# Optimization experiments

Hardware: AMD Instinct MI355X
Metric: run time of the kernel (lower is better)

The kernel has to match this reference:

```python
import jax, jax.numpy as jnp
import numpy as np


def _rope(x, token_positions, theta):
    # x: [B, H, S, D], token_positions: [S]
    d = x.shape[-1]
    freqs = 1.0 / theta ** (jnp.arange(0, d, 2, dtype=jnp.float32) / d)  # [D/2]
    angles = token_positions.astype(jnp.float32)[:, None] * freqs[None, :]  # [S, D/2]
    cos, sin = jnp.cos(angles), jnp.sin(angles)
    x_even = x[..., 0::2]
    x_odd = x[..., 1::2]
    new_even = x_even * cos - x_odd * sin
    new_odd = x_even * sin + x_odd * cos
    return jnp.stack([new_even, new_odd], axis=-1).reshape(x.shape)


def setup_inputs() -> dict:
    key = jax.random.key(0)
    ks = jax.random.split(key, 5)
    B, S, D = 2, 2048, 1024
    scale = 1.0 / np.sqrt(D)
    return {
        "x": jax.random.normal(ks[0], (B, S, D), dtype=jnp.float32),
        "Wq": jax.random.normal(ks[1], (D, D), dtype=jnp.float32) * scale,
        "Wk": jax.random.normal(ks[2], (D, D), dtype=jnp.float32) * scale,
        "Wv": jax.random.normal(ks[3], (D, D), dtype=jnp.float32) * scale,
        "Wo": jax.random.normal(ks[4], (D, D), dtype=jnp.float32) * scale,
        "token_positions": jnp.arange(S, dtype=jnp.int32),
        "rope_theta": 10000,
    }


def reference(x, Wq, Wk, Wv, Wo, token_positions, rope_theta):
    B, S, Dm = x.shape
    H = 16
    d_k = Dm // H
    # nn.Linear(bias=False): y = x @ W.T
    def proj(W):
        y = jnp.einsum('bsd,ed->bse', x, W)
        return y.reshape(B, S, H, d_k).transpose(0, 2, 1, 3)  # [B,H,S,Dk]
    q = _rope(proj(Wq), token_positions, float(rope_theta))
    k = _rope(proj(Wk), token_positions, float(rope_theta))
    v = proj(Wv)
    scores = jnp.einsum('bhqd,bhkd->bhqk', q, k) / jnp.sqrt(jnp.float32(d_k))
    causal = jnp.tril(jnp.ones((S, S), dtype=bool))
    scores = jnp.where(causal, scores, -jnp.inf)
    p = jax.nn.softmax(scores, axis=-1)
    vals = jnp.einsum('bhqk,bhkd->bhqd', p, v)
    out = vals.transpose(0, 2, 1, 3).reshape(B, S, Dm)
    return jnp.einsum('bsd,ed->bse', out, Wo)
```

## Files before the change

kernel.cpp:

```cpp
#include <hip/hip_runtime.h>
#include <hip/hip_bf16.h>
#include <stdint.h>

typedef __attribute__((ext_vector_type(8))) __bf16 bf16x8;
typedef __attribute__((ext_vector_type(4))) float f32x4;
typedef __hip_bfloat16 bf16;

#define GLDS(g, l) __builtin_amdgcn_global_load_lds( \
    (const __attribute__((address_space(1))) void*)(g), \
    (__attribute__((address_space(3))) void*)(l), 16, 0, 0)

#define SCALE_Q 0.18033688f

#define OFF_XB     ((size_t)0)
#define OFF_WQKVB  ((size_t)8388608)
#define OFF_WOB    ((size_t)14680064)
#define OFF_QB     ((size_t)16777216)
#define OFF_KB     ((size_t)25165824)
#define OFF_VTB    ((size_t)33554432)
#define OFF_CS     ((size_t)41943040)
#define OFF_SN     ((size_t)42205184)

__global__ void prep_kernel(const float* __restrict__ x, const float* __restrict__ wq,
                            const float* __restrict__ wk, const float* __restrict__ wv,
                            const float* __restrict__ wo,
                            bf16* __restrict__ xb, bf16* __restrict__ wqkvb,
                            bf16* __restrict__ wob)
{
    const int region = blockIdx.y;
    const float* src;
    bf16* dst;
    int count;
    switch (region) {
        case 0:  src = x;  dst = xb;              count = 4096 * 1024; break;
        case 1:  src = wq; dst = wqkvb;           count = 1024 * 1024; break;
        case 2:  src = wk; dst = wqkvb + 1048576; count = 1024 * 1024; break;
        case 3:  src = wv; dst = wqkvb + 2097152; count = 1024 * 1024; break;
        default: src = wo; dst = wob;             count = 1024 * 1024; break;
    }
    const int i = (blockIdx.x * 256 + threadIdx.x) * 4;
    if (i >= count) return;
    const float4 v = *(const float4*)(src + i);
    union { bf16 h[4]; short4 s4; } u;
    u.h[0] = __float2bfloat16(v.x);
    u.h[1] = __float2bfloat16(v.y);
    u.h[2] = __float2bfloat16(v.z);
    u.h[3] = __float2bfloat16(v.w);
    *(short4*)(dst + i) = u.s4;
}

__global__ void rope_table_kernel(const int* __restrict__ pos, const void* __restrict__ theta_p,
                                  float* __restrict__ cst, float* __restrict__ snt)
{
    const int t = blockIdx.x * 256 + threadIdx.x;
    const int s = t >> 5, i = t & 31;
    const int ti = ((const int*)theta_p)[0];
    const float theta = (ti > 0 && ti < 100000000) ? (float)ti : ((const float*)theta_p)[0];
    const float fr = expf(-(float)i * (1.0f / 32.0f) * logf(theta));
    const float ang = (float)pos[s] * fr;
    cst[t] = cosf(ang);
    snt[t] = sinf(ang);
}

template<int MODE, int BM>
__global__ __launch_bounds__(256) void gemm_bt(
    const bf16* __restrict__ A, const bf16* __restrict__ B,
    const int K, const int N,
    float* __restrict__ outf,
    bf16* __restrict__ qb, bf16* __restrict__ kb, bf16* __restrict__ vtb,
    const float* __restrict__ cst, const float* __restrict__ snt)
{
    constexpr int NF = BM / 32;
    __shared__ __align__(16) bf16 Asl[BM * 64];
    __shared__ __align__(16) bf16 Bsl[128 * 64];
    const int tid = threadIdx.x;
    const int wave = tid >> 6, lane = tid & 63;
    const int lr = lane & 15, lk = lane >> 4;

    const int nwg = gridDim.x * gridDim.y;
    const int flat = blockIdx.y * gridDim.x + blockIdx.x;
    const int wg = (flat & 7) * (nwg >> 3) + (flat >> 3);
    const int m0 = (wg % gridDim.x) * BM;
    const int n0 = (wg / gridDim.x) * 128;

    const int wm = (wave >> 1) * (BM / 2);
    const int wn = (wave & 1) * 64;
    const int srow = tid >> 3, sseg = tid & 7;
    const int swel = (sseg ^ (srow & 7)) * 8;

    f32x4 acc[NF][4] = {};

    const bf16* aRow = A + (size_t)(m0 + srow) * K + swel;
    const bf16* bRow = B + (size_t)(n0 + srow) * K + swel;
    char* lA = (char*)Asl + tid * 16;
    char* lB = (char*)Bsl + tid * 16;
    const size_t rowK32 = (size_t)32 * K;

    for (int k0 = 0; k0 < K; k0 += 64) {
#pragma unroll
        for (int g = 0; g < NF; ++g)
            GLDS(aRow + k0 + g * rowK32, lA + g * 4096);
#pragma unroll
        for (int g = 0; g < 4; ++g)
            GLDS(bRow + k0 + g * rowK32, lB + g * 4096);
        __syncthreads();
#pragma unroll
        for (int kk = 0; kk < 2; ++kk) {
            const int s = kk * 4 + lk;
            bf16x8 af[NF], bfr[4];
#pragma unroll
            for (int i = 0; i < NF; ++i) {
                const int R = wm + i * 16 + lr;
                af[i] = *(const bf16x8*)((const char*)Asl + R * 128 + (((s) ^ (R & 7)) << 4));
            }
#pragma unroll
            for (int j = 0; j < 4; ++j) {
                const int R = wn + j * 16 + lr;
                bfr[j] = *(const bf16x8*)((const char*)Bsl + R * 128 + (((s) ^ (R & 7)) << 4));
            }
#pragma unroll
            for (int i = 0; i < NF; ++i)
#pragma unroll
                for (int j = 0; j < 4; ++j)
                    acc[i][j] = __builtin_amdgcn_mfma_f32_16x16x32_bf16(af[i], bfr[j], acc[i][j], 0, 0, 0);
        }
        __syncthreads();
    }

    if constexpr (MODE == 1) {
#pragma unroll
        for (int i = 0; i < NF; ++i)
#pragma unroll
            for (int j = 0; j < 4; ++j)
#pragma unroll
                for (int r = 0; r < 4; ++r) {
                    const int row = m0 + wm + i * 16 + lk * 4 + r;
                    const int col = n0 + wn + j * 16 + lr;
                    outf[(size_t)row * N + col] = acc[i][j][r];
                }
    } else {
        const int matn = n0 >> 10;
#pragma unroll
        for (int i = 0; i < NF; ++i)
#pragma unroll
            for (int j = 0; j < 4; ++j)
#pragma unroll
                for (int r = 0; r < 4; ++r) {
                    const int row = m0 + wm + i * 16 + lk * 4 + r;
                    const int col = n0 + wn + j * 16 + lr;
                    float v = acc[i][j][r];
                    float p = __shfl_xor(v, 1);
                    const int e = col & 1023;
                    const int h = e >> 6;
                    const int dd = e & 63;
                    const int b = row >> 11;
                    const int s = row & 2047;
                    const size_t bhi = (size_t)(b * 16 + h);
                    if (matn == 2) {
                        vtb[(bhi * 64 + dd) * 2048 + s] = __float2bfloat16(v);
                    } else {
                        const float cs = cst[s * 32 + (dd >> 1)];
                        const float sn = snt[s * 32 + (dd >> 1)];
                        const float rv = (dd & 1) ? (p * sn + v * cs) : (v * cs - p * sn);
                        if (matn == 0)
                            qb[(bhi * 2048 + s) * 64 + dd] = __float2bfloat16(rv * SCALE_Q);
                        else
                            kb[(bhi * 2048 + s) * 64 + dd] = __float2bfloat16(rv);
                    }
                }
    }
}

__global__ __launch_bounds__(256) void attn_kernel(
    const bf16* __restrict__ qb, const bf16* __restrict__ kb,
    const bf16* __restrict__ vtb, bf16* __restrict__ attnb)
{
    __shared__ __align__(16) bf16 Kl[2][64 * 64];
    __shared__ __align__(16) bf16 Vl[2][64 * 64];
    __shared__ __align__(16) bf16 Pl[4][16][72];
    const int tid = threadIdx.x;
    const int wave = tid >> 6, lane = tid & 63;
    const int lr = lane & 15, lk = lane >> 4;
    const int tA = blockIdx.x;
    const int tB = 31 - tA;
    const int bh = blockIdx.y;
    const int qA = tA * 64 + wave * 16;
    const int qB = tB * 64 + wave * 16;

    const bf16* Qp = qb + (size_t)bh * 2048 * 64;
    const bf16* Kp = kb + (size_t)bh * 2048 * 64;
    const bf16* Vp = vtb + (size_t)bh * 64 * 2048;

    const int srow = tid >> 3;
    const int sseg = tid & 7;
    const int sw16 = (sseg ^ (srow & 7)) * 16;
    const char* kg = (const char*)Kp + (size_t)srow * 128 + sw16;
    const char* vg = (const char*)Vp + (size_t)srow * 4096 + sw16;

#define STAGE(kt_, c_) do {                                              \
        const char* kgt = kg + (size_t)(kt_) * 8192;                     \
        GLDS(kgt,              &Kl[c_][0] + tid * 8);                    \
        GLDS(kgt + 32 * 128,   &Kl[c_][0] + 2048 + tid * 8);             \
        const char* vgt = vg + (size_t)(kt_) * 128;                      \
        GLDS(vgt,              &Vl[c_][0] + tid * 8);                    \
        GLDS(vgt + 32 * 4096,  &Vl[c_][0] + 2048 + tid * 8);             \
    } while (0)

    bf16x8 qfA[2], qfB[2];
#pragma unroll
    for (int ks = 0; ks < 2; ++ks) {
        qfA[ks] = *(const bf16x8*)(Qp + (qA + lr) * 64 + ks * 32 + lk * 8);
        qfB[ks] = *(const bf16x8*)(Qp + (qB + lr) * 64 + ks * 32 + lk * 8);
    }

    float mA = -1e30f, mB = -1e30f, sA = 0.f, sB = 0.f;
    f32x4 oA[4] = {}, oB[4] = {};

    STAGE(0, 0);

    const int xoff = (lr & 7) * 8;

    for (int kt = 0; kt <= tB; ++kt) {
        const int c = kt & 1;
        const int kv0 = kt * 64;
        const bool doA = (kt <= tA);
        if (kt < tB) {
            STAGE(kt + 1, c ^ 1);
            asm volatile("s_waitcnt vmcnt(4)" ::: "memory");
        } else {
            asm volatile("s_waitcnt vmcnt(0)" ::: "memory");
        }
        __builtin_amdgcn_s_barrier();
        __builtin_amdgcn_sched_barrier(0);
        const bf16* Kc = &Kl[c][0];
        const bf16* Vc = &Vl[c][0];

        f32x4 scB[4] = {}, scA[4] = {};
#pragma unroll
        for (int ks = 0; ks < 2; ++ks) {
            bf16x8 kf[4];
#pragma unroll
            for (int j = 0; j < 4; ++j)
                kf[j] = *(const bf16x8*)(Kc + (j * 16 + lr) * 64 + ((ks * 32 + lk * 8) ^ xoff));
            __builtin_amdgcn_s_setprio(1);
#pragma unroll
            for (int j = 0; j < 4; ++j)
                scB[j] = __builtin_amdgcn_mfma_f32_16x16x32_bf16(kf[j], qfB[ks], scB[j], 0, 0, 0);
            if (doA) {
#pragma unroll
                for (int j = 0; j < 4; ++j)
                    scA[j] = __builtin_amdgcn_mfma_f32_16x16x32_bf16(kf[j], qfA[ks], scA[j], 0, 0, 0);
            }
            __builtin_amdgcn_s_setprio(0);
        }

        bf16x8 vf[2][4];
#pragma unroll
        for (int ks = 0; ks < 2; ++ks)
#pragma unroll
            for (int j = 0; j < 4; ++j)
                vf[ks][j] = *(const bf16x8*)(Vc + (j * 16 + lr) * 64 + ((ks * 32 + lk * 8) ^ xoff));

        auto smx = [&](f32x4* sc, float& m, float& ssum, f32x4* o, int qX, bool diag) {
            if (diag) {
#pragma unroll
                for (int j = 0; j < 4; ++j)
#pragma unroll
                    for (int r = 0; r < 4; ++r)
                        if (kv0 + j * 16 + lk * 4 + r > qX + lr) sc[j][r] = -1e30f;
            }
            float mt = sc[0][0];
#pragma unroll
            for (int j = 0; j < 4; ++j)
#pragma unroll
                for (int r = 0; r < 4; ++r) mt = fmaxf(mt, sc[j][r]);
            mt = fmaxf(mt, __shfl_xor(mt, 16));
            mt = fmaxf(mt, __shfl_xor(mt, 32));
            if (!__all(mt <= m + 8.0f)) {
                const float mn = fmaxf(m, mt);
                const float al = exp2f(m - mn);
                m = mn;
                ssum *= al;
#pragma unroll
                for (int j = 0; j < 4; ++j)
#pragma unroll
                    for (int r = 0; r < 4; ++r) o[j][r] *= al;
            }
            float ls = 0.f;
#pragma unroll
            for (int j = 0; j < 4; ++j) {
                float pv[4];
#pragma unroll
                for (int r = 0; r < 4; ++r) {
                    pv[r] = exp2f(sc[j][r] - m);
                    ls += pv[r];
                }
                union { bf16 h[4]; ushort4 s4; } u;
#pragma unroll
                for (int r = 0; r < 4; ++r) u.h[r] = __float2bfloat16(pv[r]);
                *(ushort4*)(&Pl[wave][lr][j * 16 + lk * 4]) = u.s4;
            }
            ssum += ls;
        };
        auto pv = [&](f32x4* o) {
#pragma unroll
            for (int ks = 0; ks < 2; ++ks) {
                const bf16x8 pf = *(const bf16x8*)(&Pl[wave][lr][ks * 32 + lk * 8]);
                __builtin_amdgcn_s_setprio(1);
#pragma unroll
                for (int j = 0; j < 4; ++j)
                    o[j] = __builtin_amdgcn_mfma_f32_16x16x32_bf16(vf[ks][j], pf, o[j], 0, 0, 0);
                __builtin_amdgcn_s_setprio(0);
            }
        };

        smx(scB, mB, sB, oB, qB, kt == tB);
        pv(oB);
        if (doA) {
            smx(scA, mA, sA, oA, qA, kt == tA);
            pv(oA);
        }
        __builtin_amdgcn_sched_barrier(0);
        __builtin_amdgcn_s_barrier();
    }

    const int b = bh >> 4, h = bh & 15;
    auto epi = [&](float ssum, f32x4* o, int qX) {
        float s = ssum;
        s += __shfl_xor(s, 16);
        s += __shfl_xor(s, 32);
        const float inv = 1.0f / s;
        const int qq = qX + lr;
        bf16* dst = attnb + (size_t)(b * 2048 + qq) * 1024 + h * 64 + lk * 4;
#pragma unroll
        for (int j = 0; j < 4; ++j) {
            union { bf16 h4[4]; ushort4 s4; } u;
#pragma unroll
            for (int r = 0; r < 4; ++r) u.h4[r] = __float2bfloat16(o[j][r] * inv);
            *(ushort4*)(dst + j * 16) = u.s4;
        }
    };
    epi(sA, oA, qA);
    epi(sB, oB, qB);
#undef STAGE
}

extern "C" void kernel_launch(void* const* d_in, const int* in_sizes, int n_in,
                              void* d_out, int out_size, void* d_ws, size_t ws_size,
                              hipStream_t stream)
{
    const float* x   = (const float*)d_in[0];
    const float* wq  = (const float*)d_in[1];
    const float* wk  = (const float*)d_in[2];
    const float* wv  = (const float*)d_in[3];
    const float* wo  = (const float*)d_in[4];
    const int*   pos = (const int*)d_in[5];
    const void* theta = d_in[6];

    char* ws = (char*)d_ws;
    bf16* xb    = (bf16*)(ws + OFF_XB);
    bf16* attnb = (bf16*)(ws + OFF_XB);
    bf16* wqkvb = (bf16*)(ws + OFF_WQKVB);
    bf16* wob   = (bf16*)(ws + OFF_WOB);
    bf16* qb    = (bf16*)(ws + OFF_QB);
    bf16* kb    = (bf16*)(ws + OFF_KB);
    bf16* vtb   = (bf16*)(ws + OFF_VTB);
    float* cst  = (float*)(ws + OFF_CS);
    float* snt  = (float*)(ws + OFF_SN);

    prep_kernel<<<dim3(4096, 5), 256, 0, stream>>>(x, wq, wk, wv, wo, xb, wqkvb, wob);
    rope_table_kernel<<<256, 256, 0, stream>>>(pos, theta, cst, snt);
    gemm_bt<0, 128><<<dim3(32, 24), 256, 0, stream>>>(xb, wqkvb, 1024, 3072, nullptr,
                                                      qb, kb, vtb, cst, snt);
    attn_kernel<<<dim3(16, 32), 256, 0, stream>>>(qb, kb, vtb, attnb);
    gemm_bt<1, 64><<<dim3(64, 8), 256, 0, stream>>>(attnb, wob, 1024, 1024, (float*)d_out,
                                                    nullptr, nullptr, nullptr, nullptr, nullptr);
}
```

Before: 144.9 us.

## Replace paired causal query tiles with one query tile per block

The attention kernel no longer pairs query tile t with tile 31-t inside one block to balance causal work. Each block now handles a single 64-row query tile, heaviest tiles first, and the grid doubles to 32x32 blocks. This gives more blocks and lower register pressure for better occupancy. In exchange, each K/V tile loaded into LDS is reused by one query tile instead of two, and per-block work becomes uneven, so balance depends on the hardware scheduler.

```diff
diff --git a/kernel.cpp b/kernel.cpp
--- a/kernel.cpp
+++ b/kernel.cpp
@@ -181,11 +181,9 @@
     const int tid = threadIdx.x;
     const int wave = tid >> 6, lane = tid & 63;
     const int lr = lane & 15, lk = lane >> 4;
-    const int tA = blockIdx.x;
-    const int tB = 31 - tA;
+    const int qt = 31 - blockIdx.x;
     const int bh = blockIdx.y;
-    const int qA = tA * 64 + wave * 16;
-    const int qB = tB * 64 + wave * 16;
+    const int qw = qt * 64 + wave * 16;
 
     const bf16* Qp = qb + (size_t)bh * 2048 * 64;
     const bf16* Kp = kb + (size_t)bh * 2048 * 64;
@@ -206,25 +204,22 @@
         GLDS(vgt + 32 * 4096,  &Vl[c_][0] + 2048 + tid * 8);             \
     } while (0)
 
-    bf16x8 qfA[2], qfB[2];
-#pragma unroll
-    for (int ks = 0; ks < 2; ++ks) {
-        qfA[ks] = *(const bf16x8*)(Qp + (qA + lr) * 64 + ks * 32 + lk * 8);
-        qfB[ks] = *(const bf16x8*)(Qp + (qB + lr) * 64 + ks * 32 + lk * 8);
-    }
-
-    float mA = -1e30f, mB = -1e30f, sA = 0.f, sB = 0.f;
-    f32x4 oA[4] = {}, oB[4] = {};
+    bf16x8 qf[2];
+#pragma unroll
+    for (int ks = 0; ks < 2; ++ks)
+        qf[ks] = *(const bf16x8*)(Qp + (qw + lr) * 64 + ks * 32 + lk * 8);
+
+    float m = -1e30f, ssum = 0.f;
+    f32x4 o[4] = {};
 
     STAGE(0, 0);
 
     const int xoff = (lr & 7) * 8;
 
-    for (int kt = 0; kt <= tB; ++kt) {
+    for (int kt = 0; kt <= qt; ++kt) {
         const int c = kt & 1;
         const int kv0 = kt * 64;
-        const bool doA = (kt <= tA);
-        if (kt < tB) {
+        if (kt < qt) {
             STAGE(kt + 1, c ^ 1);
             asm volatile("s_waitcnt vmcnt(4)" ::: "memory");
         } else {
@@ -235,7 +230,7 @@
         const bf16* Kc = &Kl[c][0];
         const bf16* Vc = &Vl[c][0];
 
-        f32x4 scB[4] = {}, scA[4] = {};
+        f32x4 sc[4] = {};
 #pragma unroll
         for (int ks = 0; ks < 2; ++ks) {
             bf16x8 kf[4];
@@ -245,92 +240,77 @@
             __builtin_amdgcn_s_setprio(1);
 #pragma unroll
             for (int j = 0; j < 4; ++j)
-                scB[j] = __builtin_amdgcn_mfma_f32_16x16x32_bf16(kf[j], qfB[ks], scB[j], 0, 0, 0);
-            if (doA) {
-#pragma unroll
-                for (int j = 0; j < 4; ++j)
-                    scA[j] = __builtin_amdgcn_mfma_f32_16x16x32_bf16(kf[j], qfA[ks], scA[j], 0, 0, 0);
+                sc[j] = __builtin_amdgcn_mfma_f32_16x16x32_bf16(kf[j], qf[ks], sc[j], 0, 0, 0);
+            __builtin_amdgcn_s_setprio(0);
+        }
+
+        bf16x8 vf[2][4];
+#pragma unroll
+        for (int ks = 0; ks < 2; ++ks)
+#pragma unroll
+            for (int j = 0; j < 4; ++j)
+                vf[ks][j] = *(const bf16x8*)(Vc + (j * 16 + lr) * 64 + ((ks * 32 + lk * 8) ^ xoff));
+
+        if (kt == qt) {
+#pragma unroll
+            for (int j = 0; j < 4; ++j)
+#pragma unroll
+                for (int r = 0; r < 4; ++r)
+                    if (kv0 + j * 16 + lk * 4 + r > qw + lr) sc[j][r] = -1e30f;
+        }
+        float mt = sc[0][0];
+#pragma unroll
+        for (int j = 0; j < 4; ++j)
+#pragma unroll
+            for (int r = 0; r < 4; ++r) mt = fmaxf(mt, sc[j][r]);
+        mt = fmaxf(mt, __shfl_xor(mt, 16));
+        mt = fmaxf(mt, __shfl_xor(mt, 32));
+        if (!__all(mt <= m + 8.0f)) {
+            const float mn = fmaxf(m, mt);
+            const float al = exp2f(m - mn);
+            m = mn;
+            ssum *= al;
+#pragma unroll
+            for (int j = 0; j < 4; ++j)
+#pragma unroll
+                for (int r = 0; r < 4; ++r) o[j][r] *= al;
+        }
+        float ls = 0.f;
+#pragma unroll
+        for (int j = 0; j < 4; ++j) {
+            float pv[4];
+#pragma unroll
+            for (int r = 0; r < 4; ++r) {
+                pv[r] = exp2f(sc[j][r] - m);
+                ls += pv[r];
             }
+            union { bf16 h[4]; ushort4 s4; } u;
+#pragma unroll
+            for (int r = 0; r < 4; ++r) u.h[r] = __float2bfloat16(pv[r]);
+            *(ushort4*)(&Pl[wave][lr][j * 16 + lk * 4]) = u.s4;
+        }
+        ssum += ls;
+
+#pragma unroll
+        for (int ks = 0; ks < 2; ++ks) {
+            const bf16x8 pf = *(const bf16x8*)(&Pl[wave][lr][ks * 32 + lk * 8]);
+            __builtin_amdgcn_s_setprio(1);
+#pragma unroll
+            for (int j = 0; j < 4; ++j)
+                o[j] = __builtin_amdgcn_mfma_f32_16x16x32_bf16(vf[ks][j], pf, o[j], 0, 0, 0);
             __builtin_amdgcn_s_setprio(0);
-        }
-
-        bf16x8 vf[2][4];
-#pragma unroll
-        for (int ks = 0; ks < 2; ++ks)
-#pragma unroll
-            for (int j = 0; j < 4; ++j)
-                vf[ks][j] = *(const bf16x8*)(Vc + (j * 16 + lr) * 64 + ((ks * 32 + lk * 8) ^ xoff));
-
-        auto smx = [&](f32x4* sc, float& m, float& ssum, f32x4* o, int qX, bool diag) {
-            if (diag) {
-#pragma unroll
-                for (int j = 0; j < 4; ++j)
-#pragma unroll
-                    for (int r = 0; r < 4; ++r)
-                        if (kv0 + j * 16 + lk * 4 + r > qX + lr) sc[j][r] = -1e30f;
-            }
-            float mt = sc[0][0];
-#pragma unroll
-            for (int j = 0; j < 4; ++j)
-#pragma unroll
-                for (int r = 0; r < 4; ++r) mt = fmaxf(mt, sc[j][r]);
-            mt = fmaxf(mt, __shfl_xor(mt, 16));
-            mt = fmaxf(mt, __shfl_xor(mt, 32));
-            if (!__all(mt <= m + 8.0f)) {
-                const float mn = fmaxf(m, mt);
-                const float al = exp2f(m - mn);
-                m = mn;
-                ssum *= al;
-#pragma unroll
-                for (int j = 0; j < 4; ++j)
-#pragma unroll
-                    for (int r = 0; r < 4; ++r) o[j][r] *= al;
-            }
-            float ls = 0.f;
-#pragma unroll
-            for (int j = 0; j < 4; ++j) {
-                float pv[4];
-#pragma unroll
-                for (int r = 0; r < 4; ++r) {
-                    pv[r] = exp2f(sc[j][r] - m);
-                    ls += pv[r];
-                }
-                union { bf16 h[4]; ushort4 s4; } u;
-#pragma unroll
-                for (int r = 0; r < 4; ++r) u.h[r] = __float2bfloat16(pv[r]);
-                *(ushort4*)(&Pl[wave][lr][j * 16 + lk * 4]) = u.s4;
-            }
-            ssum += ls;
-        };
-        auto pv = [&](f32x4* o) {
-#pragma unroll
-            for (int ks = 0; ks < 2; ++ks) {
-                const bf16x8 pf = *(const bf16x8*)(&Pl[wave][lr][ks * 32 + lk * 8]);
-                __builtin_amdgcn_s_setprio(1);
-#pragma unroll
-                for (int j = 0; j < 4; ++j)
-                    o[j] = __builtin_amdgcn_mfma_f32_16x16x32_bf16(vf[ks][j], pf, o[j], 0, 0, 0);
-                __builtin_amdgcn_s_setprio(0);
-            }
-        };
-
-        smx(scB, mB, sB, oB, qB, kt == tB);
-        pv(oB);
-        if (doA) {
-            smx(scA, mA, sA, oA, qA, kt == tA);
-            pv(oA);
         }
         __builtin_amdgcn_sched_barrier(0);
         __builtin_amdgcn_s_barrier();
     }
 
     const int b = bh >> 4, h = bh & 15;
-    auto epi = [&](float ssum, f32x4* o, int qX) {
+    {
         float s = ssum;
         s += __shfl_xor(s, 16);
         s += __shfl_xor(s, 32);
         const float inv = 1.0f / s;
-        const int qq = qX + lr;
+        const int qq = qw + lr;
         bf16* dst = attnb + (size_t)(b * 2048 + qq) * 1024 + h * 64 + lk * 4;
 #pragma unroll
         for (int j = 0; j < 4; ++j) {
@@ -339,9 +319,7 @@
             for (int r = 0; r < 4; ++r) u.h4[r] = __float2bfloat16(o[j][r] * inv);
             *(ushort4*)(dst + j * 16) = u.s4;
         }
-    };
-    epi(sA, oA, qA);
-    epi(sB, oB, qB);
+    }
 #undef STAGE
 }
 
@@ -372,7 +350,7 @@
     rope_table_kernel<<<256, 256, 0, stream>>>(pos, theta, cst, snt);
     gemm_bt<0, 128><<<dim3(32, 24), 256, 0, stream>>>(xb, wqkvb, 1024, 3072, nullptr,
                                                       qb, kb, vtb, cst, snt);
-    attn_kernel<<<dim3(16, 32), 256, 0, stream>>>(qb, kb, vtb, attnb);
+    attn_kernel<<<dim3(32, 32), 256, 0, stream>>>(qb, kb, vtb, attnb);
     gemm_bt<1, 64><<<dim3(64, 8), 256, 0, stream>>>(attnb, wob, 1024, 1024, (float*)d_out,
                                                     nullptr, nullptr, nullptr, nullptr, nullptr);
 }
```

After: 172.1 us. +18.8%, slower.
